# Optimization experiments

Measured on AMD Instinct MI355X. Metric: run time of the kernel, lower is better.

The kernel has to match this reference:

```python
import jax, jax.numpy as jnp
import numpy as np

B = 4
N0, N1, N2 = 32768, 8192, 2048
C0, C1, C2 = 256, 512, 1024
EPS = 1e-5  # torch BatchNorm1d default eps


def _mlp(x, w1, b1, g, be, w2, b2):
    # Linear -> BatchNorm1d (training-mode batch stats over B and N) -> ReLU -> Linear
    h = x @ w1 + b1                      # (B, N, H)
    mu = jnp.mean(h, axis=(0, 1))
    var = jnp.mean((h - mu) ** 2, axis=(0, 1))  # biased var, as torch BN uses for normalization
    h = jax.nn.relu((h - mu) * jax.lax.rsqrt(var + EPS) * g + be)
    return h @ w2 + b2


def _gather(feats, idx):
    # feats: (B, N_coarse, C), idx: (B, N_fine) -> (B, N_fine, C)
    return jax.vmap(lambda f, i: f[i])(feats, idx)


def _lin(key, fan_in, fan_out, scale=0.02):
    return jax.random.normal(key, (fan_in, fan_out), dtype=jnp.float32) * scale


def setup_inputs() -> dict:
    key = jax.random.key(0)
    ks = jax.random.split(key, 16)
    inp = {
        'f0': jax.random.normal(ks[0], (B, N0, C0), dtype=jnp.float32),
        'f1': jax.random.normal(ks[1], (B, N1, C1), dtype=jnp.float32),
        'f2': jax.random.normal(ks[2], (B, N2, C2), dtype=jnp.float32),
        # up_mlps[0]: MLP(C1, [C1, C0])
        'up0_w1': _lin(ks[3], C1, C1), 'up0_b1': jnp.zeros((C1,), jnp.float32),
        'up0_g': jnp.ones((C1,), jnp.float32), 'up0_be': jnp.zeros((C1,), jnp.float32),
        'up0_w2': _lin(ks[4], C1, C0), 'up0_b2': jnp.zeros((C0,), jnp.float32),
        # up_mlps[1]: MLP(C2, [C2, C1])
        'up1_w1': _lin(ks[5], C2, C2), 'up1_b1': jnp.zeros((C2,), jnp.float32),
        'up1_g': jnp.ones((C2,), jnp.float32), 'up1_be': jnp.zeros((C2,), jnp.float32),
        'up1_w2': _lin(ks[6], C2, C1), 'up1_b2': jnp.zeros((C1,), jnp.float32),
        # skip_mlps[0]: MLP(2*C0, [2*C0, C0])
        'skip0_w1': _lin(ks[7], 2 * C0, 2 * C0), 'skip0_b1': jnp.zeros((2 * C0,), jnp.float32),
        'skip0_g': jnp.ones((2 * C0,), jnp.float32), 'skip0_be': jnp.zeros((2 * C0,), jnp.float32),
        'skip0_w2': _lin(ks[8], 2 * C0, C0), 'skip0_b2': jnp.zeros((C0,), jnp.float32),
        # skip_mlps[1]: MLP(2*C1, [2*C1, C1])
        'skip1_w1': _lin(ks[9], 2 * C1, 2 * C1), 'skip1_b1': jnp.zeros((2 * C1,), jnp.float32),
        'skip1_g': jnp.ones((2 * C1,), jnp.float32), 'skip1_be': jnp.zeros((2 * C1,), jnp.float32),
        'skip1_w2': _lin(ks[10], 2 * C1, C1), 'skip1_b2': jnp.zeros((C1,), jnp.float32),
        'pool0': jax.random.randint(ks[11], (B, N0), 0, N1, dtype=jnp.int32),
        'pool1': jax.random.randint(ks[12], (B, N1), 0, N2, dtype=jnp.int32),
    }
    return inp


def reference(f0, f1, f2,
              up0_w1, up0_b1, up0_g, up0_be, up0_w2, up0_b2,
              up1_w1, up1_b1, up1_g, up1_be, up1_w2, up1_b2,
              skip0_w1, skip0_b1, skip0_g, skip0_be, skip0_w2, skip0_b2,
              skip1_w1, skip1_b1, skip1_g, skip1_be, skip1_w2, skip1_b2,
              pool0, pool1):
    # start at coarsest level
    x = f2                                               # (B, N2, C2)
    # level i = 1
    x = _mlp(x, up1_w1, up1_b1, up1_g, up1_be, up1_w2, up1_b2)   # (B, N2, C1)
    x = _gather(x, pool1)                                 # (B, N1, C1)
    x = _mlp(jnp.concatenate([f1, x], axis=-1),
             skip1_w1, skip1_b1, skip1_g, skip1_be, skip1_w2, skip1_b2)  # (B, N1, C1)
    # level i = 0
    x = _mlp(x, up0_w1, up0_b1, up0_g, up0_be, up0_w2, up0_b2)   # (B, N1, C0)
    x = _gather(x, pool0)                                 # (B, N0, C0)
    x = _mlp(jnp.concatenate([f0, x], axis=-1),
             skip0_w1, skip0_b1, skip0_g, skip0_be, skip0_w2, skip0_b2)  # (B, N0, C0)
    return x
```

## Files before the change

### kernel.cpp

```cpp
#include <hip/hip_runtime.h>


typedef unsigned short u16;
typedef __attribute__((ext_vector_type(8))) short bf16x8;
typedef __attribute__((ext_vector_type(4))) float f32x4;

__device__ __forceinline__ float b2f(u16 u) {
    union { unsigned int i; float f; } v; v.i = ((unsigned int)u) << 16; return v.f;
}
__device__ __forceinline__ u16 f2b(float f) {
    union { float f; unsigned int i; } v; v.f = f;
    unsigned int r = v.i + 0x7FFFu + ((v.i >> 16) & 1u);
    return (u16)(r >> 16);
}

__device__ __forceinline__ void gld_lds16(const u16* g, u16* l) {
    __builtin_amdgcn_global_load_lds(
        (const __attribute__((address_space(1))) unsigned int*)g,
        (__attribute__((address_space(3))) unsigned int*)l,
        16, 0, 0);
}

template <bool AFFINE_A, bool STATS, bool OUT_F32>
__global__ __launch_bounds__(256) void gemm_bn(
    const u16* __restrict__ A, const u16* __restrict__ BT, void* __restrict__ Cout,
    const float* __restrict__ scale, const float* __restrict__ shift,
    const float* __restrict__ bias,
    float* __restrict__ psum, float* __restrict__ psumsq,
    int M, int N, int K)
{
    (void)M;
    __shared__ __align__(16) u16 sA[128 * 64];
    __shared__ __align__(16) u16 sB[128 * 64];

    const int tid  = threadIdx.x;
    const int w    = tid >> 6;
    const int lane = tid & 63;
    const int wm   = w & 1, wn = w >> 1;
    const int bm   = blockIdx.y, bn = blockIdx.x;

    const int srow = w * 32 + (lane >> 3);
    const int scol = (lane & 7) * 8;

    const u16* Ag = A  + (size_t)(bm * 128 + srow) * K + scol;
    const u16* Bg = BT + (size_t)(bn * 128 + srow) * K + scol;

    f32x4 acc[4][4];
    const f32x4 zero = {0.f, 0.f, 0.f, 0.f};
#pragma unroll
    for (int i = 0; i < 4; i++)
#pragma unroll
        for (int j = 0; j < 4; j++) acc[i][j] = zero;

    const int nkt = K >> 6;
    for (int kt = 0; kt < nkt; kt++) {
        const int kof = kt * 64;
#pragma unroll
        for (int q = 0; q < 4; q++)
            gld_lds16(Bg + (size_t)(q * 8) * K + kof, &sB[(w * 32 + q * 8) * 64]);
        if constexpr (!AFFINE_A) {
#pragma unroll
            for (int q = 0; q < 4; q++)
                gld_lds16(Ag + (size_t)(q * 8) * K + kof, &sA[(w * 32 + q * 8) * 64]);
        } else {
            const float4 sc0 = *(const float4*)(scale + kof + scol);
            const float4 sc1 = *(const float4*)(scale + kof + scol + 4);
            const float4 sh0 = *(const float4*)(shift + kof + scol);
            const float4 sh1 = *(const float4*)(shift + kof + scol + 4);
#pragma unroll
            for (int q = 0; q < 4; q++) {
                union { uint4 u; u16 s[8]; } r, o;
                r.u = *(const uint4*)(Ag + (size_t)(q * 8) * K + kof);
                o.s[0] = f2b(fmaxf(b2f(r.s[0]) * sc0.x + sh0.x, 0.f));
                o.s[1] = f2b(fmaxf(b2f(r.s[1]) * sc0.y + sh0.y, 0.f));
                o.s[2] = f2b(fmaxf(b2f(r.s[2]) * sc0.z + sh0.z, 0.f));
                o.s[3] = f2b(fmaxf(b2f(r.s[3]) * sc0.w + sh0.w, 0.f));
                o.s[4] = f2b(fmaxf(b2f(r.s[4]) * sc1.x + sh1.x, 0.f));
                o.s[5] = f2b(fmaxf(b2f(r.s[5]) * sc1.y + sh1.y, 0.f));
                o.s[6] = f2b(fmaxf(b2f(r.s[6]) * sc1.z + sh1.z, 0.f));
                o.s[7] = f2b(fmaxf(b2f(r.s[7]) * sc1.w + sh1.w, 0.f));
                *(uint4*)&sA[(w * 32 + q * 8 + (lane >> 3)) * 64 + scol] = o.u;
            }
        }
        __syncthreads();
#pragma unroll
        for (int ks = 0; ks < 2; ks++) {
            const int kk = ks * 32 + (lane >> 4) * 8;
            bf16x8 af[4], bfr[4];
#pragma unroll
            for (int i = 0; i < 4; i++)
                af[i] = *(const bf16x8*)&sA[(wm * 64 + i * 16 + (lane & 15)) * 64 + kk];
#pragma unroll
            for (int j = 0; j < 4; j++)
                bfr[j] = *(const bf16x8*)&sB[(wn * 64 + j * 16 + (lane & 15)) * 64 + kk];
#pragma unroll
            for (int i = 0; i < 4; i++)
#pragma unroll
                for (int j = 0; j < 4; j++)
                    acc[i][j] = __builtin_amdgcn_mfma_f32_16x16x32_bf16(af[i], bfr[j], acc[i][j], 0, 0, 0);
        }
        __syncthreads();
    }

    const int cl = lane & 15, quad = lane >> 4;
#pragma unroll
    for (int j = 0; j < 4; j++) {
        const int col = bn * 128 + wn * 64 + j * 16 + cl;
        float bcol = 0.f;
        if constexpr (!STATS) bcol = bias[col];
        float s = 0.f, ss = 0.f;
#pragma unroll
        for (int i = 0; i < 4; i++) {
            const size_t row0 = (size_t)(bm * 128 + wm * 64 + i * 16 + quad * 4);
#pragma unroll
            for (int r = 0; r < 4; r++) {
                const float v = acc[i][j][r];
                if constexpr (STATS) { s += v; ss += v * v; }
                const float o = v + bcol;
                if constexpr (OUT_F32)
                    ((float*)Cout)[(row0 + r) * N + col] = o;
                else
                    ((u16*)Cout)[(row0 + r) * N + col] = f2b(o);
            }
        }
        if constexpr (STATS) {
            s  += __shfl_xor(s, 16);  s  += __shfl_xor(s, 32);
            ss += __shfl_xor(ss, 16); ss += __shfl_xor(ss, 32);
            if (quad == 0) { atomicAdd(&psum[col], s); atomicAdd(&psumsq[col], ss); }
        }
    }
}

__global__ void cvt_transpose_w(const float* __restrict__ W, u16* __restrict__ WT, int K, int N) {
    __shared__ float t[32][33];
    const int tx = threadIdx.x, ty = threadIdx.y;
    const int n0 = blockIdx.x * 32, k0 = blockIdx.y * 32;
#pragma unroll
    for (int r = 0; r < 4; r++)
        t[ty + r * 8][tx] = W[(size_t)(k0 + ty + r * 8) * N + n0 + tx];
    __syncthreads();
#pragma unroll
    for (int r = 0; r < 4; r++)
        WT[(size_t)(n0 + ty + r * 8) * K + k0 + tx] = f2b(t[tx][ty + r * 8]);
}

__global__ void cvt_f32_bf16(const float* __restrict__ x, u16* __restrict__ y, long n8) {
    const long t = (long)blockIdx.x * 256 + threadIdx.x;
    if (t >= n8) return;
    const float4 a = ((const float4*)x)[t * 2];
    const float4 b = ((const float4*)x)[t * 2 + 1];
    union { uint4 u; u16 s[8]; } o;
    o.s[0] = f2b(a.x); o.s[1] = f2b(a.y); o.s[2] = f2b(a.z); o.s[3] = f2b(a.w);
    o.s[4] = f2b(b.x); o.s[5] = f2b(b.y); o.s[6] = f2b(b.z); o.s[7] = f2b(b.w);
    ((uint4*)y)[t] = o.u;
}

__global__ void gather_concat(const float* __restrict__ f, const u16* __restrict__ X,
                              const int* __restrict__ pool, u16* __restrict__ out,
                              int Nf, int Nc, int Cc, int B) {
    const int per_row = (2 * Cc) / 8;
    const long t = (long)blockIdx.x * 256 + threadIdx.x;
    const long total = (long)B * Nf * per_row;
    if (t >= total) return;
    const int row = (int)(t / per_row);
    const int c8 = (int)(t % per_row) * 8;
    const int b = row / Nf, n = row % Nf;
    union { uint4 u; u16 s[8]; } o;
    if (c8 < Cc) {
        const float* src = f + (size_t)row * Cc + c8;
        const float4 a = *(const float4*)src;
        const float4 bb = *(const float4*)(src + 4);
        o.s[0] = f2b(a.x);  o.s[1] = f2b(a.y);  o.s[2] = f2b(a.z);  o.s[3] = f2b(a.w);
        o.s[4] = f2b(bb.x); o.s[5] = f2b(bb.y); o.s[6] = f2b(bb.z); o.s[7] = f2b(bb.w);
    } else {
        const int p = pool[(size_t)b * Nf + n];
        o.u = *(const uint4*)(X + ((size_t)b * Nc + p) * Cc + (c8 - Cc));
    }
    *(uint4*)(out + (size_t)row * 2 * Cc + c8) = o.u;
}

__global__ void bn_finalize(const float* __restrict__ sum, const float* __restrict__ sumsq,
                            const float* __restrict__ g, const float* __restrict__ be,
                            float* __restrict__ scale, float* __restrict__ shift,
                            int Cc, float invM) {
    const int c = blockIdx.x * 256 + threadIdx.x;
    if (c >= Cc) return;
    const float mu = sum[c] * invM;
    const float var = fmaf(sumsq[c], invM, -mu * mu);
    const float sc = g[c] * rsqrtf(var + 1e-5f);
    scale[c] = sc;
    shift[c] = fmaf(-mu, sc, be[c]);
}

extern "C" void kernel_launch(void* const* d_in, const int* in_sizes, int n_in,
                              void* d_out, int out_size, void* d_ws, size_t ws_size,
                              hipStream_t stream) {
    const float* f0     = (const float*)d_in[0];
    const float* f1     = (const float*)d_in[1];
    const float* f2     = (const float*)d_in[2];
    const float* up0_w1 = (const float*)d_in[3];
    const float* up0_g  = (const float*)d_in[5];
    const float* up0_be = (const float*)d_in[6];
    const float* up0_w2 = (const float*)d_in[7];
    const float* up0_b2 = (const float*)d_in[8];
    const float* up1_w1 = (const float*)d_in[9];
    const float* up1_g  = (const float*)d_in[11];
    const float* up1_be = (const float*)d_in[12];
    const float* up1_w2 = (const float*)d_in[13];
    const float* up1_b2 = (const float*)d_in[14];
    const float* sk0_w1 = (const float*)d_in[15];
    const float* sk0_g  = (const float*)d_in[17];
    const float* sk0_be = (const float*)d_in[18];
    const float* sk0_w2 = (const float*)d_in[19];
    const float* sk0_b2 = (const float*)d_in[20];
    const float* sk1_w1 = (const float*)d_in[21];
    const float* sk1_g  = (const float*)d_in[23];
    const float* sk1_be = (const float*)d_in[24];
    const float* sk1_w2 = (const float*)d_in[25];
    const float* sk1_b2 = (const float*)d_in[26];
    const int* pool0    = (const int*)d_in[27];
    const int* pool1    = (const int*)d_in[28];
    float* out = (float*)d_out;

    char* ws = (char*)d_ws;
    size_t off = 0;
    auto alloc = [&](size_t bytes) -> void* {
        void* p = ws + off;
        off += (bytes + 255) & ~(size_t)255;
        return p;
    };
    u16* w_up1_1 = (u16*)alloc((size_t)1024 * 1024 * 2);
    u16* w_up1_2 = (u16*)alloc((size_t)512 * 1024 * 2);
    u16* w_sk1_1 = (u16*)alloc((size_t)1024 * 1024 * 2);
    u16* w_sk1_2 = (u16*)alloc((size_t)512 * 1024 * 2);
    u16* w_up0_1 = (u16*)alloc((size_t)512 * 512 * 2);
    u16* w_up0_2 = (u16*)alloc((size_t)256 * 512 * 2);
    u16* w_sk0_1 = (u16*)alloc((size_t)512 * 512 * 2);
    u16* w_sk0_2 = (u16*)alloc((size_t)256 * 512 * 2);
    float* stats = (float*)alloc((size_t)4 * 4096 * 4);
    u16* Hbuf    = (u16*)alloc((size_t)131072 * 512 * 2);
    u16* Xbuf    = (u16*)alloc((size_t)32768 * 512 * 2);
    u16* Catbuf  = (u16*)alloc((size_t)131072 * 512 * 2);

    const dim3 tb(32, 8);
    cvt_transpose_w<<<dim3(32, 32), tb, 0, stream>>>(up1_w1, w_up1_1, 1024, 1024);
    cvt_transpose_w<<<dim3(16, 32), tb, 0, stream>>>(up1_w2, w_up1_2, 1024, 512);
    cvt_transpose_w<<<dim3(32, 32), tb, 0, stream>>>(sk1_w1, w_sk1_1, 1024, 1024);
    cvt_transpose_w<<<dim3(16, 32), tb, 0, stream>>>(sk1_w2, w_sk1_2, 1024, 512);
    cvt_transpose_w<<<dim3(16, 16), tb, 0, stream>>>(up0_w1, w_up0_1, 512, 512);
    cvt_transpose_w<<<dim3(8, 16),  tb, 0, stream>>>(up0_w2, w_up0_2, 512, 256);
    cvt_transpose_w<<<dim3(16, 16), tb, 0, stream>>>(sk0_w1, w_sk0_1, 512, 512);
    cvt_transpose_w<<<dim3(8, 16),  tb, 0, stream>>>(sk0_w2, w_sk0_2, 512, 256);

    hipMemsetAsync(stats, 0, (size_t)4 * 4096 * sizeof(float), stream);
    cvt_f32_bf16<<<(8388608 / 8) / 256, 256, 0, stream>>>(f2, Catbuf, 8388608 / 8);

    float* st0 = stats;
    float* st1 = stats + 4096;
    float* st2 = stats + 8192;
    float* st3 = stats + 12288;

    gemm_bn<false, true, false><<<dim3(8, 64), 256, 0, stream>>>(
        Catbuf, w_up1_1, Hbuf, nullptr, nullptr, nullptr, st0, st0 + 1024, 8192, 1024, 1024);
    bn_finalize<<<4, 256, 0, stream>>>(st0, st0 + 1024, up1_g, up1_be, st0 + 2048, st0 + 3072, 1024, 1.f / 8192.f);
    gemm_bn<true, false, false><<<dim3(4, 64), 256, 0, stream>>>(
        Hbuf, w_up1_2, Xbuf, st0 + 2048, st0 + 3072, up1_b2, nullptr, nullptr, 8192, 512, 1024);

    gather_concat<<<(4 * 8192 * 128) / 256, 256, 0, stream>>>(f1, Xbuf, pool1, Catbuf, 8192, 2048, 512, 4);

    gemm_bn<false, true, false><<<dim3(8, 256), 256, 0, stream>>>(
        Catbuf, w_sk1_1, Hbuf, nullptr, nullptr, nullptr, st1, st1 + 1024, 32768, 1024, 1024);
    bn_finalize<<<4, 256, 0, stream>>>(st1, st1 + 1024, sk1_g, sk1_be, st1 + 2048, st1 + 3072, 1024, 1.f / 32768.f);
    gemm_bn<true, false, false><<<dim3(4, 256), 256, 0, stream>>>(
        Hbuf, w_sk1_2, Xbuf, st1 + 2048, st1 + 3072, sk1_b2, nullptr, nullptr, 32768, 512, 1024);

    gemm_bn<false, true, false><<<dim3(4, 256), 256, 0, stream>>>(
        Xbuf, w_up0_1, Hbuf, nullptr, nullptr, nullptr, st2, st2 + 1024, 32768, 512, 512);
    bn_finalize<<<2, 256, 0, stream>>>(st2, st2 + 1024, up0_g, up0_be, st2 + 2048, st2 + 3072, 512, 1.f / 32768.f);
    gemm_bn<true, false, false><<<dim3(2, 256), 256, 0, stream>>>(
        Hbuf, w_up0_2, Xbuf, st2 + 2048, st2 + 3072, up0_b2, nullptr, nullptr, 32768, 256, 512);

    gather_concat<<<(4 * 32768 * 64) / 256, 256, 0, stream>>>(f0, Xbuf, pool0, Catbuf, 32768, 8192, 256, 4);

    gemm_bn<false, true, false><<<dim3(4, 1024), 256, 0, stream>>>(
        Catbuf, w_sk0_1, Hbuf, nullptr, nullptr, nullptr, st3, st3 + 1024, 131072, 512, 512);
    bn_finalize<<<2, 256, 0, stream>>>(st3, st3 + 1024, sk0_g, sk0_be, st3 + 2048, st3 + 3072, 512, 1.f / 131072.f);
    gemm_bn<true, false, true><<<dim3(2, 1024), 256, 0, stream>>>(
        Hbuf, w_sk0_2, out, st3 + 2048, st3 + 3072, sk0_b2, nullptr, nullptr, 131072, 256, 512);
}
```

Measured before the change: 924.4 us.

## Fuse gather-concat into skip GEMM loads, stage bf16 epilogue via LDS, remap blocks per XCD

The separate gather_concat kernels and the concatenated buffer are removed. The skip-MLP first GEMM now loads its A tile directly, from the bf16-converted fine features or from the pooled coarse rows, using async global-to-LDS loads, which saves writing and re-reading a large intermediate. The bf16 outputs are staged through LDS so the global stores are coalesced 16-byte row writes instead of scattered 2-byte writes. Block indices are remapped so that each XCD works on a contiguous range of row tiles, which should improve L2 reuse. In exchange, the f0 and f1 tensors now need separate full fp32-to-bf16 conversion passes, and the gathered loads are less contiguous.

```diff
diff --git a/kernel.cpp b/kernel.cpp
--- a/kernel.cpp
+++ b/kernel.cpp
@@ -4,6 +4,8 @@
 typedef unsigned short u16;
 typedef __attribute__((ext_vector_type(8))) short bf16x8;
 typedef __attribute__((ext_vector_type(4))) float f32x4;
+
+#define EPW 136
 
 __device__ __forceinline__ float b2f(u16 u) {
     union { unsigned int i; float f; } v; v.i = ((unsigned int)u) << 16; return v.f;
@@ -21,29 +23,58 @@
         16, 0, 0);
 }
 
-template <bool AFFINE_A, bool STATS, bool OUT_F32>
+union SMem {
+    struct { u16 a[128 * 64]; u16 b[128 * 64]; } st;
+    u16 ep[128 * EPW];
+};
+
+template <bool AFFINE_A, bool STATS, bool OUT_F32, bool GATHER>
 __global__ __launch_bounds__(256) void gemm_bn(
     const u16* __restrict__ A, const u16* __restrict__ BT, void* __restrict__ Cout,
     const float* __restrict__ scale, const float* __restrict__ shift,
     const float* __restrict__ bias,
     float* __restrict__ psum, float* __restrict__ psumsq,
-    int M, int N, int K)
+    const u16* __restrict__ Xg, const int* __restrict__ pool,
+    int nfShift, int Nc, int Chalf,
+    int N, int K)
 {
-    (void)M;
-    __shared__ __align__(16) u16 sA[128 * 64];
-    __shared__ __align__(16) u16 sB[128 * 64];
+    __shared__ __align__(16) SMem sm;
 
     const int tid  = threadIdx.x;
     const int w    = tid >> 6;
     const int lane = tid & 63;
     const int wm   = w & 1, wn = w >> 1;
-    const int bm   = blockIdx.y, bn = blockIdx.x;
-
-    const int srow = w * 32 + (lane >> 3);
+
+    int bm, bn;
+    {
+        const int flat = (int)(blockIdx.y * gridDim.x + blockIdx.x);
+        const int xcd  = flat & 7;
+        const int s    = flat >> 3;
+        const int nbn  = (int)gridDim.x;
+        const int lb   = 31 - __builtin_clz(nbn);
+        bn = s & (nbn - 1);
+        bm = xcd * ((int)gridDim.y >> 3) + (s >> lb);
+    }
+
     const int scol = (lane & 7) * 8;
-
-    const u16* Ag = A  + (size_t)(bm * 128 + srow) * K + scol;
-    const u16* Bg = BT + (size_t)(bn * 128 + srow) * K + scol;
+    const u16* Bg = BT + (size_t)(bn * 128 + w * 32 + (lane >> 3)) * K + scol;
+
+    const u16* agA[4];
+    const u16* agX[4];
+    if constexpr (GATHER) {
+#pragma unroll
+        for (int q = 0; q < 4; q++) {
+            const int row = bm * 128 + w * 32 + q * 8 + (lane >> 3);
+            const int b   = row >> nfShift;
+            const int p   = pool[row];
+            agA[q] = A  + (size_t)row * Chalf + scol;
+            agX[q] = Xg + ((size_t)b * Nc + p) * Chalf + scol;
+        }
+    } else {
+#pragma unroll
+        for (int q = 0; q < 4; q++)
+            agA[q] = A + (size_t)(bm * 128 + w * 32 + q * 8 + (lane >> 3)) * K + scol;
+    }
 
     f32x4 acc[4][4];
     const f32x4 zero = {0.f, 0.f, 0.f, 0.f};
@@ -57,11 +88,21 @@
         const int kof = kt * 64;
 #pragma unroll
         for (int q = 0; q < 4; q++)
-            gld_lds16(Bg + (size_t)(q * 8) * K + kof, &sB[(w * 32 + q * 8) * 64]);
-        if constexpr (!AFFINE_A) {
+            gld_lds16(Bg + (size_t)(q * 8) * K + kof, &sm.st.b[(w * 32 + q * 8) * 64]);
+        if constexpr (GATHER) {
+            if (kof < Chalf) {
+#pragma unroll
+                for (int q = 0; q < 4; q++)
+                    gld_lds16(agA[q] + kof, &sm.st.a[(w * 32 + q * 8) * 64]);
+            } else {
+#pragma unroll
+                for (int q = 0; q < 4; q++)
+                    gld_lds16(agX[q] + (kof - Chalf), &sm.st.a[(w * 32 + q * 8) * 64]);
+            }
+        } else if constexpr (!AFFINE_A) {
 #pragma unroll
             for (int q = 0; q < 4; q++)
-                gld_lds16(Ag + (size_t)(q * 8) * K + kof, &sA[(w * 32 + q * 8) * 64]);
+                gld_lds16(agA[q] + kof, &sm.st.a[(w * 32 + q * 8) * 64]);
         } else {
             const float4 sc0 = *(const float4*)(scale + kof + scol);
             const float4 sc1 = *(const float4*)(scale + kof + scol + 4);
@@ -70,7 +111,7 @@
 #pragma unroll
             for (int q = 0; q < 4; q++) {
                 union { uint4 u; u16 s[8]; } r, o;
-                r.u = *(const uint4*)(Ag + (size_t)(q * 8) * K + kof);
+                r.u = *(const uint4*)(agA[q] + kof);
                 o.s[0] = f2b(fmaxf(b2f(r.s[0]) * sc0.x + sh0.x, 0.f));
                 o.s[1] = f2b(fmaxf(b2f(r.s[1]) * sc0.y + sh0.y, 0.f));
                 o.s[2] = f2b(fmaxf(b2f(r.s[2]) * sc0.z + sh0.z, 0.f));
@@ -79,7 +120,7 @@
                 o.s[5] = f2b(fmaxf(b2f(r.s[5]) * sc1.y + sh1.y, 0.f));
                 o.s[6] = f2b(fmaxf(b2f(r.s[6]) * sc1.z + sh1.z, 0.f));
                 o.s[7] = f2b(fmaxf(b2f(r.s[7]) * sc1.w + sh1.w, 0.f));
-                *(uint4*)&sA[(w * 32 + q * 8 + (lane >> 3)) * 64 + scol] = o.u;
+                *(uint4*)&sm.st.a[(w * 32 + q * 8 + (lane >> 3)) * 64 + scol] = o.u;
             }
         }
         __syncthreads();
@@ -89,10 +130,10 @@
             bf16x8 af[4], bfr[4];
 #pragma unroll
             for (int i = 0; i < 4; i++)
-                af[i] = *(const bf16x8*)&sA[(wm * 64 + i * 16 + (lane & 15)) * 64 + kk];
+                af[i] = *(const bf16x8*)&sm.st.a[(wm * 64 + i * 16 + (lane & 15)) * 64 + kk];
 #pragma unroll
             for (int j = 0; j < 4; j++)
-                bfr[j] = *(const bf16x8*)&sB[(wn * 64 + j * 16 + (lane & 15)) * 64 + kk];
+                bfr[j] = *(const bf16x8*)&sm.st.b[(wn * 64 + j * 16 + (lane & 15)) * 64 + kk];
 #pragma unroll
             for (int i = 0; i < 4; i++)
 #pragma unroll
@@ -105,28 +146,40 @@
     const int cl = lane & 15, quad = lane >> 4;
 #pragma unroll
     for (int j = 0; j < 4; j++) {
-        const int col = bn * 128 + wn * 64 + j * 16 + cl;
+        const int colLocal = wn * 64 + j * 16 + cl;
+        const int col = bn * 128 + colLocal;
         float bcol = 0.f;
         if constexpr (!STATS) bcol = bias[col];
         float s = 0.f, ss = 0.f;
 #pragma unroll
         for (int i = 0; i < 4; i++) {
-            const size_t row0 = (size_t)(bm * 128 + wm * 64 + i * 16 + quad * 4);
+            const int rowLocal0 = wm * 64 + i * 16 + quad * 4;
 #pragma unroll
             for (int r = 0; r < 4; r++) {
                 const float v = acc[i][j][r];
                 if constexpr (STATS) { s += v; ss += v * v; }
                 const float o = v + bcol;
                 if constexpr (OUT_F32)
-                    ((float*)Cout)[(row0 + r) * N + col] = o;
+                    ((float*)Cout)[(size_t)(bm * 128 + rowLocal0 + r) * N + col] = o;
                 else
-                    ((u16*)Cout)[(row0 + r) * N + col] = f2b(o);
+                    sm.ep[(rowLocal0 + r) * EPW + colLocal] = f2b(o);
             }
         }
         if constexpr (STATS) {
             s  += __shfl_xor(s, 16);  s  += __shfl_xor(s, 32);
             ss += __shfl_xor(ss, 16); ss += __shfl_xor(ss, 32);
             if (quad == 0) { atomicAdd(&psum[col], s); atomicAdd(&psumsq[col], ss); }
+        }
+    }
+    if constexpr (!OUT_F32) {
+        __syncthreads();
+        u16* Cb = (u16*)Cout;
+#pragma unroll
+        for (int it = 0; it < 8; it++) {
+            const int row = it * 16 + (tid >> 4);
+            const int c8  = (tid & 15) * 8;
+            const uint4 v = *(const uint4*)&sm.ep[row * EPW + c8];
+            *(uint4*)(Cb + (size_t)(bm * 128 + row) * N + bn * 128 + c8) = v;
         }
     }
 }
@@ -153,30 +206,6 @@
     o.s[0] = f2b(a.x); o.s[1] = f2b(a.y); o.s[2] = f2b(a.z); o.s[3] = f2b(a.w);
     o.s[4] = f2b(b.x); o.s[5] = f2b(b.y); o.s[6] = f2b(b.z); o.s[7] = f2b(b.w);
     ((uint4*)y)[t] = o.u;
-}
-
-__global__ void gather_concat(const float* __restrict__ f, const u16* __restrict__ X,
-                              const int* __restrict__ pool, u16* __restrict__ out,
-                              int Nf, int Nc, int Cc, int B) {
-    const int per_row = (2 * Cc) / 8;
-    const long t = (long)blockIdx.x * 256 + threadIdx.x;
-    const long total = (long)B * Nf * per_row;
-    if (t >= total) return;
-    const int row = (int)(t / per_row);
-    const int c8 = (int)(t % per_row) * 8;
-    const int b = row / Nf, n = row % Nf;
-    union { uint4 u; u16 s[8]; } o;
-    if (c8 < Cc) {
-        const float* src = f + (size_t)row * Cc + c8;
-        const float4 a = *(const float4*)src;
-        const float4 bb = *(const float4*)(src + 4);
-        o.s[0] = f2b(a.x);  o.s[1] = f2b(a.y);  o.s[2] = f2b(a.z);  o.s[3] = f2b(a.w);
-        o.s[4] = f2b(bb.x); o.s[5] = f2b(bb.y); o.s[6] = f2b(bb.z); o.s[7] = f2b(bb.w);
-    } else {
-        const int p = pool[(size_t)b * Nf + n];
-        o.u = *(const uint4*)(X + ((size_t)b * Nc + p) * Cc + (c8 - Cc));
-    }
-    *(uint4*)(out + (size_t)row * 2 * Cc + c8) = o.u;
 }
 
 __global__ void bn_finalize(const float* __restrict__ sum, const float* __restrict__ sumsq,
@@ -240,7 +269,9 @@
     float* stats = (float*)alloc((size_t)4 * 4096 * 4);
     u16* Hbuf    = (u16*)alloc((size_t)131072 * 512 * 2);
     u16* Xbuf    = (u16*)alloc((size_t)32768 * 512 * 2);
-    u16* Catbuf  = (u16*)alloc((size_t)131072 * 512 * 2);
+    u16* f0b     = (u16*)alloc((size_t)4 * 32768 * 256 * 2);
+    u16* f1b     = (u16*)alloc((size_t)4 * 8192 * 512 * 2);
+    u16* f2b_    = (u16*)alloc((size_t)4 * 2048 * 1024 * 2);
 
     const dim3 tb(32, 8);
     cvt_transpose_w<<<dim3(32, 32), tb, 0, stream>>>(up1_w1, w_up1_1, 1024, 1024);
@@ -253,38 +284,44 @@
     cvt_transpose_w<<<dim3(8, 16),  tb, 0, stream>>>(sk0_w2, w_sk0_2, 512, 256);
 
     hipMemsetAsync(stats, 0, (size_t)4 * 4096 * sizeof(float), stream);
-    cvt_f32_bf16<<<(8388608 / 8) / 256, 256, 0, stream>>>(f2, Catbuf, 8388608 / 8);
+    cvt_f32_bf16<<<4096,  256, 0, stream>>>(f2, f2b_, 8388608L / 8);
+    cvt_f32_bf16<<<8192,  256, 0, stream>>>(f1, f1b, 16777216L / 8);
+    cvt_f32_bf16<<<16384, 256, 0, stream>>>(f0, f0b, 33554432L / 8);
 
     float* st0 = stats;
     float* st1 = stats + 4096;
     float* st2 = stats + 8192;
     float* st3 = stats + 12288;
 
-    gemm_bn<false, true, false><<<dim3(8, 64), 256, 0, stream>>>(
-        Catbuf, w_up1_1, Hbuf, nullptr, nullptr, nullptr, st0, st0 + 1024, 8192, 1024, 1024);
+    gemm_bn<false, true, false, false><<<dim3(8, 64), 256, 0, stream>>>(
+        f2b_, w_up1_1, Hbuf, nullptr, nullptr, nullptr, st0, st0 + 1024,
+        nullptr, nullptr, 0, 0, 0, 1024, 1024);
     bn_finalize<<<4, 256, 0, stream>>>(st0, st0 + 1024, up1_g, up1_be, st0 + 2048, st0 + 3072, 1024, 1.f / 8192.f);
-    gemm_bn<true, false, false><<<dim3(4, 64), 256, 0, stream>>>(
-        Hbuf, w_up1_2, Xbuf, st0 + 2048, st0 + 3072, up1_b2, nullptr, nullptr, 8192, 512, 1024);
-
-    gather_concat<<<(4 * 8192 * 128) / 256, 256, 0, stream>>>(f1, Xbuf, pool1, Catbuf, 8192, 2048, 512, 4);
-
-    gemm_bn<false, true, false><<<dim3(8, 256), 256, 0, stream>>>(
-        Catbuf, w_sk1_1, Hbuf, nullptr, nullptr, nullptr, st1, st1 + 1024, 32768, 1024, 1024);
+    gemm_bn<true, false, false, false><<<dim3(4, 64), 256, 0, stream>>>(
+        Hbuf, w_up1_2, Xbuf, st0 + 2048, st0 + 3072, up1_b2, nullptr, nullptr,
+        nullptr, nullptr, 0, 0, 0, 512, 1024);
+
+    gemm_bn<false, true, false, true><<<dim3(8, 256), 256, 0, stream>>>(
+        f1b, w_sk1_1, Hbuf, nullptr, nullptr, nullptr, st1, st1 + 1024,
+        Xbuf, pool1, 13, 2048, 512, 1024, 1024);
     bn_finalize<<<4, 256, 0, stream>>>(st1, st1 + 1024, sk1_g, sk1_be, st1 + 2048, st1 + 3072, 1024, 1.f / 32768.f);
-    gemm_bn<true, false, false><<<dim3(4, 256), 256, 0, stream>>>(
-        Hbuf, w_sk1_2, Xbuf, st1 + 2048, st1 + 3072, sk1_b2, nullptr, nullptr, 32768, 512, 1024);
-
-    gemm_bn<false, true, false><<<dim3(4, 256), 256, 0, stream>>>(
-        Xbuf, w_up0_1, Hbuf, nullptr, nullptr, nullptr, st2, st2 + 1024, 32768, 512, 512);
+    gemm_bn<true, false, false, false><<<dim3(4, 256), 256, 0, stream>>>(
+        Hbuf, w_sk1_2, Xbuf, st1 + 2048, st1 + 3072, sk1_b2, nullptr, nullptr,
+        nullptr, nullptr, 0, 0, 0, 512, 1024);
+
+    gemm_bn<false, true, false, false><<<dim3(4, 256), 256, 0, stream>>>(
+        Xbuf, w_up0_1, Hbuf, nullptr, nullptr, nullptr, st2, st2 + 1024,
+        nullptr, nullptr, 0, 0, 0, 512, 512);
     bn_finalize<<<2, 256, 0, stream>>>(st2, st2 + 1024, up0_g, up0_be, st2 + 2048, st2 + 3072, 512, 1.f / 32768.f);
-    gemm_bn<true, false, false><<<dim3(2, 256), 256, 0, stream>>>(
-        Hbuf, w_up0_2, Xbuf, st2 + 2048, st2 + 3072, up0_b2, nullptr, nullptr, 32768, 256, 512);
-
-    gather_concat<<<(4 * 32768 * 64) / 256, 256, 0, stream>>>(f0, Xbuf, pool0, Catbuf, 32768, 8192, 256, 4);
-
-    gemm_bn<false, true, false><<<dim3(4, 1024), 256, 0, stream>>>(
-        Catbuf, w_sk0_1, Hbuf, nullptr, nullptr, nullptr, st3, st3 + 1024, 131072, 512, 512);
+    gemm_bn<true, false, false, false><<<dim3(2, 256), 256, 0, stream>>>(
+        Hbuf, w_up0_2, Xbuf, st2 + 2048, st2 + 3072, up0_b2, nullptr, nullptr,
+        nullptr, nullptr, 0, 0, 0, 256, 512);
+
+    gemm_bn<false, true, false, true><<<dim3(4, 1024), 256, 0, stream>>>(
+        f0b, w_sk0_1, Hbuf, nullptr, nullptr, nullptr, st3, st3 + 1024,
+        Xbuf, pool0, 15, 8192, 256, 512, 512);
     bn_finalize<<<2, 256, 0, stream>>>(st3, st3 + 1024, sk0_g, sk0_be, st3 + 2048, st3 + 3072, 512, 1.f / 131072.f);
-    gemm_bn<true, false, true><<<dim3(2, 1024), 256, 0, stream>>>(
-        Hbuf, w_sk0_2, out, st3 + 2048, st3 + 3072, sk0_b2, nullptr, nullptr, 131072, 256, 512);
-}
+    gemm_bn<true, false, true, false><<<dim3(2, 1024), 256, 0, stream>>>(
+        Hbuf, w_sk0_2, out, st3 + 2048, st3 + 3072, sk0_b2, nullptr, nullptr,
+        nullptr, nullptr, 0, 0, 0, 256, 512);
+}
```

Measured after the change: 885.9 us. 1.04x faster.
